# Performance work log

Measured on AMD Instinct MI355X. Metric: run time of the kernel, lower is better.

The kernel has to match this reference:

```python
import jax, jax.numpy as jnp
import numpy as np

B, T, D, H = 4, 2048, 256, 8
HD = D // H  # head_dim = 32
ALPHA_INIT = 0.5


def setup_inputs() -> dict:
    key = jax.random.key(0)
    ks = jax.random.split(key, 9)
    s = 1.0 / np.sqrt(D)
    inp = {
        "content": jax.random.normal(ks[0], (B, T, D), dtype=jnp.float32),
        "category": jax.random.normal(ks[1], (B, T, D), dtype=jnp.float32),
        "Wqc": jax.random.normal(ks[2], (D, D), dtype=jnp.float32) * s,
        "Wkc": jax.random.normal(ks[3], (D, D), dtype=jnp.float32) * s,
        "Wv": jax.random.normal(ks[4], (D, D), dtype=jnp.float32) * s,
        "Wqk": jax.random.normal(ks[5], (D, D), dtype=jnp.float32) * s,
        "Wkk": jax.random.normal(ks[6], (D, D), dtype=jnp.float32) * s,
        "Wo": jax.random.normal(ks[7], (D, D), dtype=jnp.float32) * s,
        "bo": jnp.zeros((D,), dtype=jnp.float32),
        "alpha_logit": jnp.float32(np.log(ALPHA_INIT / (1.0 - ALPHA_INIT))),
        "causal_mask": jnp.triu(jnp.ones((T, T), dtype=bool), k=1),  # True = blocked
    }
    return inp


def _split_heads(x):
    # [B, T, D] -> [B, H, T, HD]
    b, t, _ = x.shape
    return x.reshape(b, t, H, HD).transpose(0, 2, 1, 3)


def reference(content, category, Wqc, Wkc, Wv, Wqk, Wkk, Wo, bo, alpha_logit, causal_mask):
    scale = HD ** (-0.5)
    # torch nn.Linear(bias=False): y = x @ W.T
    Qc = _split_heads(content @ Wqc.T)
    Kc = _split_heads(content @ Wkc.T)
    V = _split_heads(content @ Wv.T)
    Qk = _split_heads(category @ Wqk.T)
    Kk = _split_heads(category @ Wkk.T)

    neg_inf = jnp.finfo(content.dtype).min
    Ac = jnp.einsum("bhqd,bhkd->bhqk", Qc, Kc) * scale
    Ak = jnp.einsum("bhqd,bhkd->bhqk", Qk, Kk) * scale
    Ac = jnp.where(causal_mask, neg_inf, Ac)
    Ak = jnp.where(causal_mask, neg_inf, Ak)
    Ac = jax.nn.softmax(Ac, axis=-1)
    Ak = jax.nn.softmax(Ak, axis=-1)

    alpha = jax.nn.sigmoid(alpha_logit)
    A = alpha * Ak + (1.0 - alpha) * Ac  # dropout is identity in eval mode

    out = jnp.einsum("bhqk,bhkd->bhqd", A, V)
    out = out.transpose(0, 2, 1, 3).reshape(content.shape[0], -1, D)
    return out @ Wo.T + bo
```

## Files before the change

### kernel.cpp

```cpp
#include <hip/hip_runtime.h>
#include <hip/hip_bf16.h>

#define Bb 4
#define Tt 2048
#define Dd 256
#define Hh 8
#define Mm (Bb * Tt)
#define BUFE ((unsigned)Mm * Dd)

#define QC_OFF 0u
#define KC_OFF (1u * BUFE)
#define VT_OFF (2u * BUFE)
#define QK_OFF (3u * BUFE)
#define KK_OFF (4u * BUFE)
#define AO_OFF (5u * BUFE)

typedef __attribute__((ext_vector_type(8))) short short8v;
typedef __attribute__((ext_vector_type(4))) short short4v;
typedef __attribute__((ext_vector_type(4))) float f32x4;
typedef __attribute__((ext_vector_type(4))) unsigned uint4v;

#define MFMA16(a, b, c) __builtin_amdgcn_mfma_f32_16x16x32_bf16(a, b, c, 0, 0, 0)

__device__ __forceinline__ void gload16(const void* g, void* l) {
  __builtin_amdgcn_global_load_lds((const __attribute__((address_space(1))) void*)g,
                                   (__attribute__((address_space(3))) void*)l, 16, 0, 0);
}

__device__ __forceinline__ short bfc(float f) {
  __hip_bfloat16 h = __float2bfloat16(f);
  return *reinterpret_cast<short*>(&h);
}
__device__ __forceinline__ unsigned pk2bf(float lo, float hi) {
  union { float f; unsigned u; } a, b; a.f = lo; b.f = hi;
  return __builtin_amdgcn_perm(b.u, a.u, 0x07060302u);
}

__global__ __launch_bounds__(256)
void proj_kernel(const float* __restrict__ content, const float* __restrict__ category,
                 const float* __restrict__ Wqc, const float* __restrict__ Wkc,
                 const float* __restrict__ Wv, const float* __restrict__ Wqk,
                 const float* __restrict__ Wkk, short* __restrict__ ws) {
  __shared__ short Al[128][40];
  __shared__ short Bl[128][40];

  const int mt = blockIdx.x;
  const int nt = blockIdx.y;
  const int p  = nt >> 1;
  const int n0 = (nt & 1) << 7;

  const float* X = (p < 3) ? content : category;
  const float* W = (p == 0) ? Wqc : (p == 1) ? Wkc : (p == 2) ? Wv : (p == 3) ? Wqk : Wkk;
  short* Y = ws + (size_t)p * ((size_t)Mm * Dd);
  const float oscale = (p == 0 || p == 3)
      ? (0.17677669529663689f * 1.4426950408889634f) : 1.0f;

  const int tid  = threadIdx.x;
  const int lane = tid & 63;
  const int wv   = tid >> 6;
  const int wm   = (wv >> 1) << 6;
  const int wn   = (wv & 1) << 6;
  const int l15  = lane & 15;
  const int l4   = lane >> 4;

  const f32x4 zero = {0.f, 0.f, 0.f, 0.f};
  f32x4 acc[4][4];
#pragma unroll
  for (int i = 0; i < 4; i++)
#pragma unroll
    for (int j = 0; j < 4; j++) acc[i][j] = zero;

  const int rs = tid >> 3;
  const int cs = (tid & 7) << 2;

  for (int k0 = 0; k0 < Dd; k0 += 32) {
#pragma unroll
    for (int pass = 0; pass < 4; pass++) {
      const int r = rs + (pass << 5);
      const float4 va = *reinterpret_cast<const float4*>(&X[(size_t)(mt * 128 + r) * Dd + k0 + cs]);
      short4v sa; sa[0] = bfc(va.x); sa[1] = bfc(va.y); sa[2] = bfc(va.z); sa[3] = bfc(va.w);
      *reinterpret_cast<short4v*>(&Al[r][cs]) = sa;
      const float4 vb = *reinterpret_cast<const float4*>(&W[(size_t)(n0 + r) * Dd + k0 + cs]);
      short4v sb; sb[0] = bfc(vb.x); sb[1] = bfc(vb.y); sb[2] = bfc(vb.z); sb[3] = bfc(vb.w);
      *reinterpret_cast<short4v*>(&Bl[r][cs]) = sb;
    }
    __syncthreads();

    short8v af[4], bfr[4];
#pragma unroll
    for (int i = 0; i < 4; i++)
      af[i] = *reinterpret_cast<const short8v*>(&Al[wm + i * 16 + l15][l4 * 8]);
#pragma unroll
    for (int j = 0; j < 4; j++)
      bfr[j] = *reinterpret_cast<const short8v*>(&Bl[wn + j * 16 + l15][l4 * 8]);
#pragma unroll
    for (int i = 0; i < 4; i++)
#pragma unroll
      for (int j = 0; j < 4; j++)
        acc[i][j] = MFMA16(af[i], bfr[j], acc[i][j]);
    __syncthreads();
  }

  if (p == 2) {
#pragma unroll
    for (int i = 0; i < 4; i++) {
      const int trow = mt * 128 + wm + i * 16 + (l4 << 2);
      const int bidx = trow >> 11;
      const int tloc = trow & 2047;
#pragma unroll
      for (int j = 0; j < 4; j++) {
        const int cg = n0 + wn + j * 16 + l15;
        const int hh = cg >> 5, dd2 = cg & 31;
        short4v pk;
#pragma unroll
        for (int e = 0; e < 4; e++) pk[e] = bfc(acc[i][j][e]);
        *reinterpret_cast<short4v*>(&Y[((size_t)(bidx * 8 + hh) * 32 + dd2) * Tt + tloc]) = pk;
      }
    }
  } else {
#pragma unroll
    for (int i = 0; i < 4; i++) {
      const int rb = mt * 128 + wm + i * 16 + (l4 << 2);
#pragma unroll
      for (int j = 0; j < 4; j++) {
        const int c = n0 + wn + j * 16 + l15;
#pragma unroll
        for (int e = 0; e < 4; e++)
          Y[(size_t)(rb + e) * Dd + c] = bfc(acc[i][j][e] * oscale);
      }
    }
  }
}

__global__ __launch_bounds__(512, 4)
void attn_kernel(const short* __restrict__ ws, const float* __restrict__ alpha_p) {
  __shared__ __align__(16) char ldsraw[49152];

  const int bid = blockIdx.x;
  const int bh  = bid & 31;
  const int qt  = 31 - (bid >> 5);
  const int b = bh >> 3, h = bh & 7;
  const unsigned rowbase = (unsigned)b * Tt;

  const int tid  = threadIdx.x;
  const int lane = tid & 63;
  const int grp  = tid >> 8;
  const int tg   = tid & 255;
  const int wq   = (tid >> 6) & 3;
  const int l15  = lane & 15, g = lane >> 4;

  char* gb = ldsraw + grp * 24576;

  const int slot = tg >> 2;
  const int ksrc = ((slot >> 4) & 1) * 32 + ((slot >> 2) & 3) * 8
                 + (slot >> 5) * 4 + (slot & 3);
  const int kcg  = (tg & 3) ^ ((slot >> 1) & 3);
  const int vrow = tg >> 3;
  const int vcg  = (tg & 7) ^ (vrow & 7);

  const int koff  = l15 * 32 + ((g ^ ((l15 >> 1) & 3)) << 3);
  const int voff0 = l15 * 64 + (((g) ^ (l15 & 7)) << 3);

  const float alpha = 1.f / (1.f + __builtin_amdgcn_exp2f(-alpha_p[0] * 1.4426950408889634f));
  const f32x4 zf = {0.f, 0.f, 0.f, 0.f};

  const unsigned qIdx = (rowbase + (unsigned)(qt << 6) + wq * 16 + l15) * Dd + h * 32 + g * 8;
  const short8v qcf = *(const short8v*)&ws[QC_OFF + qIdx];
  const short8v qkf = *(const short8v*)&ws[QK_OFF + qIdx];

  f32x4 ov[2][2];
  float ls[2] = {0.f, 0.f};
#pragma unroll
  for (int s = 0; s < 2; s++) { ov[s][0] = zf; ov[s][1] = zf; }

  const unsigned kIdx0 = (rowbase + (unsigned)ksrc) * Dd + h * 32 + kcg * 8;
  const unsigned vIdx0 = ((unsigned)bh * 32 + vrow) * Tt + vcg * 8;

  {
    const unsigned kI = kIdx0 + (unsigned)(grp << 6) * Dd;
    const unsigned vI = vIdx0 + (unsigned)(grp << 6);
    gload16(ws + (KC_OFF + kI), gb + wq * 1024);
    gload16(ws + (KK_OFF + kI), gb + 8192 + wq * 1024);
    gload16(ws + (VT_OFF + vI), gb + 16384 + wq * 1024);
  }
  __syncthreads();

  unsigned kPf = kIdx0 + (unsigned)((grp + 2) << 6) * Dd;
  unsigned vPf = vIdx0 + (unsigned)((grp + 2) << 6);

  const int nIter = (qt >> 1) + 1;
  int jt = grp;
  for (int it = 0; it < nIter; ++it, jt += 2) {
    const int cur = it & 1;
    if (jt + 2 <= qt) {
      char* db = gb + (cur ^ 1) * 4096 + wq * 1024;
      gload16(ws + (KC_OFF + kPf), db);
      gload16(ws + (KK_OFF + kPf), db + 8192);
      gload16(ws + (VT_OFF + vPf), db + 16384);
      kPf += 128u * Dd; vPf += 128u;
    }
    if (jt <= qt) {
      const short* kcl = (const short*)(gb + cur * 4096);
      const short* kkl = (const short*)(gb + 8192 + cur * 4096);
      const short* vtl = (const short*)(gb + 16384 + cur * 4096);

      const short8v vb00 = *(const short8v*)(vtl + voff0);
      const short8v vb10 = *(const short8v*)(vtl + voff0 + 1024);
      const short8v vb01 = *(const short8v*)(vtl + (voff0 ^ 32));
      const short8v vb11 = *(const short8v*)(vtl + (voff0 ^ 32) + 1024);

      const bool diag = (jt == qt);
      const bool full = !diag || (wq >= 2);
#pragma unroll
      for (int s = 0; s < 2; s++) {
        const short* kl = s ? kkl : kcl;
        const short8v qf = s ? qkf : qcf;
        f32x4 sf[4];
#pragma unroll
        for (int f = 0; f < 4; f++) {
          if (((f & 1) == 0) || full) {
            const short8v kf = *(const short8v*)(kl + koff + f * 512);
            sf[f] = MFMA16(kf, qf, zf);
          }
        }
        if (diag) {
          const int thb = 16 * wq + l15 - 8 * g;
#pragma unroll
          for (int f = 0; f < 4; f++) {
            if (((f & 1) == 0) || full) {
              const int thr = thb - 32 * (f & 1) - 4 * (f >> 1);
#pragma unroll
              for (int e = 0; e < 4; e++)
                if (e > thr) sf[f][e] = -1e30f;
            }
          }
        }
#pragma unroll
        for (int f = 0; f < 4; f++) {
          if (((f & 1) == 0) || full) {
#pragma unroll
            for (int e = 0; e < 4; e++)
              sf[f][e] = __builtin_amdgcn_exp2f(sf[f][e]);
          }
        }
        const float t0 = (sf[0][0] + sf[0][1]) + (sf[0][2] + sf[0][3]);
        const float t2 = (sf[2][0] + sf[2][1]) + (sf[2][2] + sf[2][3]);
        float ts = t0 + t2;
        if (full) {
          const float t1 = (sf[1][0] + sf[1][1]) + (sf[1][2] + sf[1][3]);
          const float t3 = (sf[3][0] + sf[3][1]) + (sf[3][2] + sf[3][3]);
          ts += (t1 + t3);
        }
        ts += __shfl_xor(ts, 16);
        ts += __shfl_xor(ts, 32);
        ls[s] += ts;

        union { uint4v u; short8v s8; } pa;
        pa.u = (uint4v){pk2bf(sf[0][0], sf[0][1]), pk2bf(sf[0][2], sf[0][3]),
                        pk2bf(sf[2][0], sf[2][1]), pk2bf(sf[2][2], sf[2][3])};
        __builtin_amdgcn_s_setprio(1);
        ov[s][0] = MFMA16(pa.s8, vb00, ov[s][0]);
        ov[s][1] = MFMA16(pa.s8, vb10, ov[s][1]);
        __builtin_amdgcn_s_setprio(0);
        if (full) {
          pa.u = (uint4v){pk2bf(sf[1][0], sf[1][1]), pk2bf(sf[1][2], sf[1][3]),
                          pk2bf(sf[3][0], sf[3][1]), pk2bf(sf[3][2], sf[3][3])};
          __builtin_amdgcn_s_setprio(1);
          ov[s][0] = MFMA16(pa.s8, vb01, ov[s][0]);
          ov[s][1] = MFMA16(pa.s8, vb11, ov[s][1]);
          __builtin_amdgcn_s_setprio(0);
        }
      }
    }
    __syncthreads();
  }

  float* sp = (float*)ldsraw + (size_t)(wq * 64 + lane) * 20;
  if (grp == 1) {
#pragma unroll
    for (int s = 0; s < 2; s++) {
      *(f32x4*)(sp + s * 8)     = ov[s][0];
      *(f32x4*)(sp + s * 8 + 4) = ov[s][1];
    }
    sp[16] = ls[0]; sp[17] = ls[1];
  }
  __syncthreads();
  if (grp == 0) {
#pragma unroll
    for (int s = 0; s < 2; s++) {
      ov[s][0] += *(const f32x4*)(sp + s * 8);
      ov[s][1] += *(const f32x4*)(sp + s * 8 + 4);
    }
    const float l0 = ls[0] + sp[16];
    const float l1 = ls[1] + sp[17];
    float r0[4], r1[4];
#pragma unroll
    for (int e = 0; e < 4; e++) {
      r0[e] = (1.f - alpha) / __shfl(l0, 4 * g + e);
      r1[e] = alpha / __shfl(l1, 4 * g + e);
    }
    const unsigned orow = rowbase + (unsigned)(qt << 6) + wq * 16 + g * 4;
#pragma unroll
    for (int n = 0; n < 2; n++)
#pragma unroll
      for (int e = 0; e < 4; e++) {
        const float o = ov[0][n][e] * r0[e] + ov[1][n][e] * r1[e];
        *(short*)(ws + (AO_OFF + (orow + e) * Dd + h * 32 + n * 16 + l15)) = bfc(o);
      }
  }
}

__global__ __launch_bounds__(256)
void outproj_kernel(const short* __restrict__ AO, const float* __restrict__ Wo,
                    const float* __restrict__ bo, float* __restrict__ out) {
  __shared__ short Al[64][40];
  __shared__ short Bl[64][40];

  const int mt = blockIdx.x;
  const int n0 = (int)blockIdx.y << 6;

  const int tid  = threadIdx.x;
  const int lane = tid & 63;
  const int wv   = tid >> 6;
  const int wm   = (wv >> 1) << 5;
  const int wn   = (wv & 1) << 5;
  const int l15  = lane & 15;
  const int g    = lane >> 4;

  const f32x4 zero = {0.f, 0.f, 0.f, 0.f};
  f32x4 acc[2][2] = {{zero, zero}, {zero, zero}};

  const int ra = tid >> 2, ca = (tid & 3) << 3;
  const int rb = tid >> 3, cb = (tid & 7) << 2;

  for (int k0 = 0; k0 < Dd; k0 += 32) {
    *reinterpret_cast<short8v*>(&Al[ra][ca]) =
        *reinterpret_cast<const short8v*>(&AO[(size_t)(mt * 64 + ra) * Dd + k0 + ca]);
#pragma unroll
    for (int pass = 0; pass < 2; pass++) {
      const int r = rb + (pass << 5);
      const float4 vb = *reinterpret_cast<const float4*>(&Wo[(size_t)(n0 + r) * Dd + k0 + cb]);
      short4v sb; sb[0] = bfc(vb.x); sb[1] = bfc(vb.y); sb[2] = bfc(vb.z); sb[3] = bfc(vb.w);
      *reinterpret_cast<short4v*>(&Bl[r][cb]) = sb;
    }
    __syncthreads();

    short8v af[2], bf2[2];
#pragma unroll
    for (int i = 0; i < 2; i++)
      af[i] = *reinterpret_cast<const short8v*>(&Al[wm + i * 16 + l15][g * 8]);
#pragma unroll
    for (int j = 0; j < 2; j++)
      bf2[j] = *reinterpret_cast<const short8v*>(&Bl[wn + j * 16 + l15][g * 8]);
#pragma unroll
    for (int i = 0; i < 2; i++)
#pragma unroll
      for (int j = 0; j < 2; j++)
        acc[i][j] = MFMA16(af[i], bf2[j], acc[i][j]);
    __syncthreads();
  }

#pragma unroll
  for (int i = 0; i < 2; i++) {
    const int r0w = mt * 64 + wm + i * 16 + (g << 2);
#pragma unroll
    for (int j = 0; j < 2; j++) {
      const int c = n0 + wn + j * 16 + l15;
      const float bias = bo[c];
#pragma unroll
      for (int e = 0; e < 4; e++)
        out[(size_t)(r0w + e) * Dd + c] = acc[i][j][e] + bias;
    }
  }
}

extern "C" void kernel_launch(void* const* d_in, const int* in_sizes, int n_in,
                              void* d_out, int out_size, void* d_ws, size_t ws_size,
                              hipStream_t stream) {
  const float* content = (const float*)d_in[0];
  const float* category = (const float*)d_in[1];
  const float* Wqc = (const float*)d_in[2];
  const float* Wkc = (const float*)d_in[3];
  const float* Wv  = (const float*)d_in[4];
  const float* Wqk = (const float*)d_in[5];
  const float* Wkk = (const float*)d_in[6];
  const float* Wo  = (const float*)d_in[7];
  const float* bo  = (const float*)d_in[8];
  const float* alpha_logit = (const float*)d_in[9];
  float* out = (float*)d_out;

  short* ws = (short*)d_ws;
  short* AO = ws + 5 * (size_t)BUFE;

  proj_kernel<<<dim3(64, 10), 256, 0, stream>>>(content, category, Wqc, Wkc, Wv, Wqk, Wkk, ws);
  attn_kernel<<<dim3(1024), 512, 0, stream>>>(ws, alpha_logit);
  outproj_kernel<<<dim3(128, 4), 256, 0, stream>>>(AO, Wo, bo, out);
}
```

Measured before the change: 69.25 us.

## Shrink projection tiles to 64x64 and drop intra-block KV split in attention

The projection GEMM moves from 128x128 to 64x64 tiles with a transposed grid, giving 2560 blocks instead of 640 to fill more CUs. The attention kernel drops its two 256-thread groups that split key tiles (even/odd) and reduced partial results through LDS. It now uses a single 256-thread group that walks all key tiles with double buffering, which halves LDS per block and allows more resident blocks. The cost is less parallelism per query tile and more redundant global loads in the GEMM.

New measurement: 82.61 us. +19.3%, slower.

```diff
diff --git a/kernel.cpp b/kernel.cpp
--- a/kernel.cpp
+++ b/kernel.cpp
@@ -41,13 +41,13 @@
                  const float* __restrict__ Wqc, const float* __restrict__ Wkc,
                  const float* __restrict__ Wv, const float* __restrict__ Wqk,
                  const float* __restrict__ Wkk, short* __restrict__ ws) {
-  __shared__ short Al[128][40];
-  __shared__ short Bl[128][40];
-
-  const int mt = blockIdx.x;
-  const int nt = blockIdx.y;
-  const int p  = nt >> 1;
-  const int n0 = (nt & 1) << 7;
+  __shared__ short Al[64][40];
+  __shared__ short Bl[64][40];
+
+  const int nt = blockIdx.x;
+  const int mt = blockIdx.y;
+  const int p  = nt >> 2;
+  const int n0 = (nt & 3) << 6;
 
   const float* X = (p < 3) ? content : category;
   const float* W = (p == 0) ? Wqc : (p == 1) ? Wkc : (p == 2) ? Wv : (p == 3) ? Wqk : Wkk;
@@ -58,26 +58,22 @@
   const int tid  = threadIdx.x;
   const int lane = tid & 63;
   const int wv   = tid >> 6;
-  const int wm   = (wv >> 1) << 6;
-  const int wn   = (wv & 1) << 6;
+  const int wm   = (wv >> 1) << 5;
+  const int wn   = (wv & 1) << 5;
   const int l15  = lane & 15;
   const int l4   = lane >> 4;
 
   const f32x4 zero = {0.f, 0.f, 0.f, 0.f};
-  f32x4 acc[4][4];
-#pragma unroll
-  for (int i = 0; i < 4; i++)
-#pragma unroll
-    for (int j = 0; j < 4; j++) acc[i][j] = zero;
+  f32x4 acc[2][2] = {{zero, zero}, {zero, zero}};
 
   const int rs = tid >> 3;
   const int cs = (tid & 7) << 2;
 
   for (int k0 = 0; k0 < Dd; k0 += 32) {
 #pragma unroll
-    for (int pass = 0; pass < 4; pass++) {
+    for (int pass = 0; pass < 2; pass++) {
       const int r = rs + (pass << 5);
-      const float4 va = *reinterpret_cast<const float4*>(&X[(size_t)(mt * 128 + r) * Dd + k0 + cs]);
+      const float4 va = *reinterpret_cast<const float4*>(&X[(size_t)(mt * 64 + r) * Dd + k0 + cs]);
       short4v sa; sa[0] = bfc(va.x); sa[1] = bfc(va.y); sa[2] = bfc(va.z); sa[3] = bfc(va.w);
       *reinterpret_cast<short4v*>(&Al[r][cs]) = sa;
       const float4 vb = *reinterpret_cast<const float4*>(&W[(size_t)(n0 + r) * Dd + k0 + cs]);
@@ -86,29 +82,29 @@
     }
     __syncthreads();
 
-    short8v af[4], bfr[4];
-#pragma unroll
-    for (int i = 0; i < 4; i++)
+    short8v af[2], bfr[2];
+#pragma unroll
+    for (int i = 0; i < 2; i++)
       af[i] = *reinterpret_cast<const short8v*>(&Al[wm + i * 16 + l15][l4 * 8]);
 #pragma unroll
-    for (int j = 0; j < 4; j++)
+    for (int j = 0; j < 2; j++)
       bfr[j] = *reinterpret_cast<const short8v*>(&Bl[wn + j * 16 + l15][l4 * 8]);
 #pragma unroll
-    for (int i = 0; i < 4; i++)
-#pragma unroll
-      for (int j = 0; j < 4; j++)
+    for (int i = 0; i < 2; i++)
+#pragma unroll
+      for (int j = 0; j < 2; j++)
         acc[i][j] = MFMA16(af[i], bfr[j], acc[i][j]);
     __syncthreads();
   }
 
   if (p == 2) {
 #pragma unroll
-    for (int i = 0; i < 4; i++) {
-      const int trow = mt * 128 + wm + i * 16 + (l4 << 2);
+    for (int i = 0; i < 2; i++) {
+      const int trow = mt * 64 + wm + i * 16 + (l4 << 2);
       const int bidx = trow >> 11;
       const int tloc = trow & 2047;
 #pragma unroll
-      for (int j = 0; j < 4; j++) {
+      for (int j = 0; j < 2; j++) {
         const int cg = n0 + wn + j * 16 + l15;
         const int hh = cg >> 5, dd2 = cg & 31;
         short4v pk;
@@ -119,10 +115,10 @@
     }
   } else {
 #pragma unroll
-    for (int i = 0; i < 4; i++) {
-      const int rb = mt * 128 + wm + i * 16 + (l4 << 2);
-#pragma unroll
-      for (int j = 0; j < 4; j++) {
+    for (int i = 0; i < 2; i++) {
+      const int rb = mt * 64 + wm + i * 16 + (l4 << 2);
+#pragma unroll
+      for (int j = 0; j < 2; j++) {
         const int c = n0 + wn + j * 16 + l15;
 #pragma unroll
         for (int e = 0; e < 4; e++)
@@ -132,9 +128,9 @@
   }
 }
 
-__global__ __launch_bounds__(512, 4)
+__global__ __launch_bounds__(256, 8)
 void attn_kernel(const short* __restrict__ ws, const float* __restrict__ alpha_p) {
-  __shared__ __align__(16) char ldsraw[49152];
+  __shared__ __align__(16) char ldsraw[24576];
 
   const int bid = blockIdx.x;
   const int bh  = bid & 31;
@@ -144,19 +140,15 @@
 
   const int tid  = threadIdx.x;
   const int lane = tid & 63;
-  const int grp  = tid >> 8;
-  const int tg   = tid & 255;
-  const int wq   = (tid >> 6) & 3;
+  const int wq   = tid >> 6;
   const int l15  = lane & 15, g = lane >> 4;
 
-  char* gb = ldsraw + grp * 24576;
-
-  const int slot = tg >> 2;
+  const int slot = tid >> 2;
   const int ksrc = ((slot >> 4) & 1) * 32 + ((slot >> 2) & 3) * 8
                  + (slot >> 5) * 4 + (slot & 3);
-  const int kcg  = (tg & 3) ^ ((slot >> 1) & 3);
-  const int vrow = tg >> 3;
-  const int vcg  = (tg & 7) ^ (vrow & 7);
+  const int kcg  = (tid & 3) ^ ((slot >> 1) & 3);
+  const int vrow = tid >> 3;
+  const int vcg  = (tid & 7) ^ (vrow & 7);
 
   const int koff  = l15 * 32 + ((g ^ ((l15 >> 1) & 3)) << 3);
   const int voff0 = l15 * 64 + (((g) ^ (l15 & 7)) << 3);
@@ -176,33 +168,27 @@
   const unsigned kIdx0 = (rowbase + (unsigned)ksrc) * Dd + h * 32 + kcg * 8;
   const unsigned vIdx0 = ((unsigned)bh * 32 + vrow) * Tt + vcg * 8;
 
-  {
-    const unsigned kI = kIdx0 + (unsigned)(grp << 6) * Dd;
-    const unsigned vI = vIdx0 + (unsigned)(grp << 6);
-    gload16(ws + (KC_OFF + kI), gb + wq * 1024);
-    gload16(ws + (KK_OFF + kI), gb + 8192 + wq * 1024);
-    gload16(ws + (VT_OFF + vI), gb + 16384 + wq * 1024);
-  }
+  gload16(ws + (KC_OFF + kIdx0), ldsraw + wq * 1024);
+  gload16(ws + (KK_OFF + kIdx0), ldsraw + 8192 + wq * 1024);
+  gload16(ws + (VT_OFF + vIdx0), ldsraw + 16384 + wq * 1024);
   __syncthreads();
 
-  unsigned kPf = kIdx0 + (unsigned)((grp + 2) << 6) * Dd;
-  unsigned vPf = vIdx0 + (unsigned)((grp + 2) << 6);
-
-  const int nIter = (qt >> 1) + 1;
-  int jt = grp;
-  for (int it = 0; it < nIter; ++it, jt += 2) {
-    const int cur = it & 1;
-    if (jt + 2 <= qt) {
-      char* db = gb + (cur ^ 1) * 4096 + wq * 1024;
+  unsigned kPf = kIdx0 + 64u * Dd;
+  unsigned vPf = vIdx0 + 64u;
+
+  for (int jt = 0; jt <= qt; ++jt) {
+    const int cur = jt & 1;
+    if (jt < qt) {
+      char* db = ldsraw + (cur ^ 1) * 4096 + wq * 1024;
       gload16(ws + (KC_OFF + kPf), db);
       gload16(ws + (KK_OFF + kPf), db + 8192);
       gload16(ws + (VT_OFF + vPf), db + 16384);
-      kPf += 128u * Dd; vPf += 128u;
-    }
-    if (jt <= qt) {
-      const short* kcl = (const short*)(gb + cur * 4096);
-      const short* kkl = (const short*)(gb + 8192 + cur * 4096);
-      const short* vtl = (const short*)(gb + 16384 + cur * 4096);
+      kPf += 64u * Dd; vPf += 64u;
+    }
+    {
+      const short* kcl = (const short*)(ldsraw + cur * 4096);
+      const short* kkl = (const short*)(ldsraw + 8192 + cur * 4096);
+      const short* vtl = (const short*)(ldsraw + 16384 + cur * 4096);
 
       const short8v vb00 = *(const short8v*)(vtl + voff0);
       const short8v vb10 = *(const short8v*)(vtl + voff0 + 1024);
@@ -275,39 +261,20 @@
     __syncthreads();
   }
 
-  float* sp = (float*)ldsraw + (size_t)(wq * 64 + lane) * 20;
-  if (grp == 1) {
-#pragma unroll
-    for (int s = 0; s < 2; s++) {
-      *(f32x4*)(sp + s * 8)     = ov[s][0];
-      *(f32x4*)(sp + s * 8 + 4) = ov[s][1];
-    }
-    sp[16] = ls[0]; sp[17] = ls[1];
-  }
-  __syncthreads();
-  if (grp == 0) {
-#pragma unroll
-    for (int s = 0; s < 2; s++) {
-      ov[s][0] += *(const f32x4*)(sp + s * 8);
-      ov[s][1] += *(const f32x4*)(sp + s * 8 + 4);
-    }
-    const float l0 = ls[0] + sp[16];
-    const float l1 = ls[1] + sp[17];
-    float r0[4], r1[4];
+  float r0[4], r1[4];
+#pragma unroll
+  for (int e = 0; e < 4; e++) {
+    r0[e] = (1.f - alpha) / __shfl(ls[0], 4 * g + e);
+    r1[e] = alpha / __shfl(ls[1], 4 * g + e);
+  }
+  const unsigned orow = rowbase + (unsigned)(qt << 6) + wq * 16 + g * 4;
+#pragma unroll
+  for (int n = 0; n < 2; n++)
 #pragma unroll
     for (int e = 0; e < 4; e++) {
-      r0[e] = (1.f - alpha) / __shfl(l0, 4 * g + e);
-      r1[e] = alpha / __shfl(l1, 4 * g + e);
-    }
-    const unsigned orow = rowbase + (unsigned)(qt << 6) + wq * 16 + g * 4;
-#pragma unroll
-    for (int n = 0; n < 2; n++)
-#pragma unroll
-      for (int e = 0; e < 4; e++) {
-        const float o = ov[0][n][e] * r0[e] + ov[1][n][e] * r1[e];
-        *(short*)(ws + (AO_OFF + (orow + e) * Dd + h * 32 + n * 16 + l15)) = bfc(o);
-      }
-  }
+      const float o = ov[0][n][e] * r0[e] + ov[1][n][e] * r1[e];
+      *(short*)(ws + (AO_OFF + (orow + e) * Dd + h * 32 + n * 16 + l15)) = bfc(o);
+    }
 }
 
 __global__ __launch_bounds__(256)
@@ -392,7 +359,7 @@
   short* ws = (short*)d_ws;
   short* AO = ws + 5 * (size_t)BUFE;
 
-  proj_kernel<<<dim3(64, 10), 256, 0, stream>>>(content, category, Wqc, Wkc, Wv, Wqk, Wkk, ws);
-  attn_kernel<<<dim3(1024), 512, 0, stream>>>(ws, alpha_logit);
+  proj_kernel<<<dim3(20, 128), 256, 0, stream>>>(content, category, Wqc, Wkc, Wv, Wqk, Wkk, ws);
+  attn_kernel<<<dim3(1024), 256, 0, stream>>>(ws, alpha_logit);
   outproj_kernel<<<dim3(128, 4), 256, 0, stream>>>(AO, Wo, bo, out);
 }
```

## Triple-buffer K/V tile loads with partial vmcnt waits in attention loop

Applied to the files above, without the earlier changes.

Moves the attention kernel's K/V staging from double to triple buffering, so two tiles are in flight ahead of compute. The full __syncthreads at the end of each iteration becomes an explicit s_waitcnt vmcnt(3) plus a barrier, so only the oldest loads must land before the barrier. Out-of-range prefetches are clamped to the diagonal tile, which turns them into redundant loads rather than skipped ones. LDS per block grows from 48KB to 72KB, which may reduce how many blocks fit per CU.

Result: no change. 69.27 us (+0.0%).

```diff
diff --git a/kernel.cpp b/kernel.cpp
--- a/kernel.cpp
+++ b/kernel.cpp
@@ -134,7 +134,7 @@
 
 __global__ __launch_bounds__(512, 4)
 void attn_kernel(const short* __restrict__ ws, const float* __restrict__ alpha_p) {
-  __shared__ __align__(16) char ldsraw[49152];
+  __shared__ __align__(16) char ldsraw[73728];
 
   const int bid = blockIdx.x;
   const int bh  = bid & 31;
@@ -149,7 +149,7 @@
   const int wq   = (tid >> 6) & 3;
   const int l15  = lane & 15, g = lane >> 4;
 
-  char* gb = ldsraw + grp * 24576;
+  char* gb = ldsraw + grp * 36864;
 
   const int slot = tg >> 2;
   const int ksrc = ((slot >> 4) & 1) * 32 + ((slot >> 2) & 3) * 8
@@ -176,33 +176,31 @@
   const unsigned kIdx0 = (rowbase + (unsigned)ksrc) * Dd + h * 32 + kcg * 8;
   const unsigned vIdx0 = ((unsigned)bh * 32 + vrow) * Tt + vcg * 8;
 
-  {
-    const unsigned kI = kIdx0 + (unsigned)(grp << 6) * Dd;
-    const unsigned vI = vIdx0 + (unsigned)(grp << 6);
-    gload16(ws + (KC_OFF + kI), gb + wq * 1024);
-    gload16(ws + (KK_OFF + kI), gb + 8192 + wq * 1024);
-    gload16(ws + (VT_OFF + vI), gb + 16384 + wq * 1024);
-  }
-  __syncthreads();
-
-  unsigned kPf = kIdx0 + (unsigned)((grp + 2) << 6) * Dd;
-  unsigned vPf = vIdx0 + (unsigned)((grp + 2) << 6);
+  auto stage = [&](int buf, int jwant) {
+    const int js = (jwant < qt) ? jwant : qt;
+    const unsigned kI = kIdx0 + ((unsigned)js << 14);
+    const unsigned vI = vIdx0 + ((unsigned)js << 6);
+    char* db = gb + buf * 4096 + wq * 1024;
+    gload16(ws + (KC_OFF + kI), db);
+    gload16(ws + (KK_OFF + kI), db + 12288);
+    gload16(ws + (VT_OFF + vI), db + 24576);
+  };
+
+  stage(0, grp);
+  stage(1, grp + 2);
+  asm volatile("s_waitcnt vmcnt(3) lgkmcnt(0)" ::: "memory");
+  __builtin_amdgcn_s_barrier();
+  __builtin_amdgcn_sched_barrier(0);
 
   const int nIter = (qt >> 1) + 1;
+  int cur = 0, stg = 2;
   int jt = grp;
   for (int it = 0; it < nIter; ++it, jt += 2) {
-    const int cur = it & 1;
-    if (jt + 2 <= qt) {
-      char* db = gb + (cur ^ 1) * 4096 + wq * 1024;
-      gload16(ws + (KC_OFF + kPf), db);
-      gload16(ws + (KK_OFF + kPf), db + 8192);
-      gload16(ws + (VT_OFF + vPf), db + 16384);
-      kPf += 128u * Dd; vPf += 128u;
-    }
+    stage(stg, jt + 4);
     if (jt <= qt) {
       const short* kcl = (const short*)(gb + cur * 4096);
-      const short* kkl = (const short*)(gb + 8192 + cur * 4096);
-      const short* vtl = (const short*)(gb + 16384 + cur * 4096);
+      const short* kkl = (const short*)(gb + 12288 + cur * 4096);
+      const short* vtl = (const short*)(gb + 24576 + cur * 4096);
 
       const short8v vb00 = *(const short8v*)(vtl + voff0);
       const short8v vb10 = *(const short8v*)(vtl + voff0 + 1024);
@@ -272,8 +270,14 @@
         }
       }
     }
-    __syncthreads();
-  }
+    asm volatile("s_waitcnt vmcnt(3) lgkmcnt(0)" ::: "memory");
+    __builtin_amdgcn_s_barrier();
+    __builtin_amdgcn_sched_barrier(0);
+    cur = (cur == 2) ? 0 : cur + 1;
+    stg = (stg == 2) ? 0 : stg + 1;
+  }
+
+  __syncthreads();
 
   float* sp = (float*)ldsraw + (size_t)(wq * 64 + lane) * 20;
   if (grp == 1) {
```
